# Kernel optimization log

Hardware: AMD Instinct MI355X
Metric: run time of the kernel (lower is better)

Reference implementation:

```python
import jax, jax.numpy as jnp
import numpy as np

P = 2048
D = 1024
H = 16
DH = D // H
HID = 32


def setup_inputs() -> dict:
    key = jax.random.key(0)
    ks = jax.random.split(key, 10)
    s = 0.02
    return {
        "x": jax.random.normal(ks[0], (P, D), jnp.float32),
        "rel": jax.random.normal(ks[1], (P, P, 2), jnp.float32),
        "w_qkv": jax.random.normal(ks[2], (D, 3 * D), jnp.float32) * s,
        "w_proj": jax.random.normal(ks[3], (D, D), jnp.float32) * s,
        "rpb_w1": jax.random.normal(ks[4], (2, HID), jnp.float32) * s,
        "rpb_b1": jnp.zeros((HID,), jnp.float32),
        "rpb_w2": jax.random.normal(ks[5], (HID, HID), jnp.float32) * s,
        "rpb_b2": jnp.zeros((HID,), jnp.float32),
        "rpb_w3": jax.random.normal(ks[6], (HID, 1), jnp.float32) * s,
        "rpb_b3": jnp.zeros((1,), jnp.float32),
    }


def reference(x, rel, w_qkv, w_proj, rpb_w1, rpb_b1, rpb_w2, rpb_b2, rpb_w3, rpb_b3):
    scale = 1.0 / np.sqrt(DH)
    qkv = x @ w_qkv                                   # [P, 3D]
    q, k, v = jnp.split(qkv, 3, axis=-1)
    # [P, D] -> [H, P, DH]
    q = q.reshape(P, H, DH).transpose(1, 0, 2)
    k = k.reshape(P, H, DH).transpose(1, 0, 2)
    v = v.reshape(P, H, DH).transpose(1, 0, 2)
    logits = jnp.einsum('hpd,hqd->hpq', q, k) * scale  # [H, P, P]
    # RelPosBias MLP: (dx,dy) -> scalar, applied over [P, P, 2]
    hcur = jax.nn.relu(rel @ rpb_w1 + rpb_b1)
    hcur = jax.nn.relu(hcur @ rpb_w2 + rpb_b2)
    bias = (hcur @ rpb_w3 + rpb_b3)[..., 0]            # [P, P]
    logits = logits + bias[None]
    attn = jax.nn.softmax(logits, axis=-1)
    out = jnp.einsum('hpq,hqd->hpd', attn, v)          # [H, P, DH]
    out = out.transpose(1, 0, 2).reshape(P, D)
    return out @ w_proj
```

## Files before the change

kernel.cpp:

```cpp
#include <hip/hip_runtime.h>
#include <hip/hip_bf16.h>
#include <type_traits>

typedef __attribute__((ext_vector_type(8))) short bf16x8;
typedef __attribute__((ext_vector_type(4))) float floatx4;
typedef __attribute__((ext_vector_type(2))) float float2v;

__device__ __forceinline__ float bf2f(unsigned short u) {
    union { unsigned int x; float f; } v; v.x = ((unsigned int)u) << 16; return v.f;
}
__device__ __forceinline__ unsigned short f2bf(float f) {
    union { float f; unsigned int u; } v; v.f = f;
    unsigned int x = v.u;
    unsigned int r = x + 0x7fffu + ((x >> 16) & 1u);
    return (unsigned short)(r >> 16);
}

typedef const __attribute__((address_space(1))) unsigned int u32_g;
typedef __attribute__((address_space(3))) unsigned int u32_l;
__device__ __forceinline__ void gld_lds16(const void* g, void* l) {
    __builtin_amdgcn_global_load_lds((u32_g*)g, (u32_l*)l, 16, 0, 0);
}

__device__ __forceinline__ void trans32(const float* __restrict__ in,
                                        unsigned short* __restrict__ out,
                                        int K, int N, int bx, int by,
                                        unsigned short (*T)[33]) {
    const int n0 = bx * 32, k0 = by * 32;
    const int r = threadIdx.x >> 3;
    const int c4 = (threadIdx.x & 7) * 4;
    float4 v = *reinterpret_cast<const float4*>(in + (size_t)(k0 + r) * N + n0 + c4);
    T[c4 + 0][r] = f2bf(v.x);
    T[c4 + 1][r] = f2bf(v.y);
    T[c4 + 2][r] = f2bf(v.z);
    T[c4 + 3][r] = f2bf(v.w);
    __syncthreads();
    ushort4 o = {T[r][c4], T[r][c4 + 1], T[r][c4 + 2], T[r][c4 + 3]};
    *reinterpret_cast<ushort4*>(out + (size_t)(n0 + r) * K + k0 + c4) = o;
}

__global__ __launch_bounds__(256) void prep(const float* __restrict__ x,
                                            unsigned short* __restrict__ xb,
                                            const float* __restrict__ wq,
                                            unsigned short* __restrict__ wqT,
                                            const float* __restrict__ wp,
                                            unsigned short* __restrict__ wpT) {
    __shared__ unsigned short T[32][33];
    const int b = blockIdx.x;
    if (b < 1024) {
        size_t i = ((size_t)b * 256 + threadIdx.x) * 8;
        float4 a = *reinterpret_cast<const float4*>(x + i);
        float4 c = *reinterpret_cast<const float4*>(x + i + 4);
        unsigned short t[8] = {f2bf(a.x), f2bf(a.y), f2bf(a.z), f2bf(a.w),
                               f2bf(c.x), f2bf(c.y), f2bf(c.z), f2bf(c.w)};
        *reinterpret_cast<uint4*>(xb + i) = *reinterpret_cast<const uint4*>(t);
    } else if (b < 4096) {
        int t = b - 1024;
        trans32(wq, wqT, 1024, 3072, t % 96, t / 96, T);
    } else {
        int t = b - 4096;
        trans32(wp, wpT, 1024, 1024, t % 32, t / 32, T);
    }
}

__device__ __forceinline__ void gemm128_body(const unsigned short* __restrict__ A,
                                             const unsigned short* __restrict__ Bt,
                                             unsigned short* __restrict__ C,
                                             int bx, int by,
                                             unsigned short* As, unsigned short* Bs) {
    const int tid = threadIdx.x;
    const int wave = tid >> 6;
    const int lane = tid & 63;
    const int m15 = lane & 15;
    const int quad = lane >> 4;
    const int wm = wave >> 1;
    const int wn = wave & 1;
    const int m0 = by * 128;
    const int n0 = bx * 128;
    const int srow = lane >> 2;
    const int scol = (lane & 3) * 8;

    floatx4 acc[4][4];
#pragma unroll
    for (int mt = 0; mt < 4; mt++)
#pragma unroll
        for (int nt = 0; nt < 4; nt++) acc[mt][nt] = {0.f, 0.f, 0.f, 0.f};

    for (int k0 = 0; k0 < 1024; k0 += 32) {
#pragma unroll
        for (int i = 0; i < 2; i++) {
            int j = wave * 2 + i;
            gld_lds16(A + (size_t)(m0 + j * 16 + srow) * 1024 + k0 + scol, &As[j * 16 * 32]);
            gld_lds16(Bt + (size_t)(n0 + j * 16 + srow) * 1024 + k0 + scol, &Bs[j * 16 * 32]);
        }
        __syncthreads();

        bf16x8 a[4];
#pragma unroll
        for (int mt = 0; mt < 4; mt++)
            a[mt] = *reinterpret_cast<bf16x8*>(&As[(wm * 64 + mt * 16 + m15) * 32 + quad * 8]);
#pragma unroll
        for (int nt = 0; nt < 4; nt++) {
            bf16x8 b = *reinterpret_cast<bf16x8*>(&Bs[(wn * 64 + nt * 16 + m15) * 32 + quad * 8]);
#pragma unroll
            for (int mt = 0; mt < 4; mt++)
                acc[mt][nt] = __builtin_amdgcn_mfma_f32_16x16x32_bf16(a[mt], b, acc[mt][nt], 0, 0, 0);
        }
        __syncthreads();
    }

#pragma unroll
    for (int mt = 0; mt < 4; mt++)
#pragma unroll
        for (int nt = 0; nt < 4; nt++)
#pragma unroll
            for (int i = 0; i < 4; i++) {
                int row = m0 + wm * 64 + mt * 16 + quad * 4 + i;
                int col = n0 + wn * 64 + nt * 16 + m15;
                C[(size_t)row * 3072 + col] = f2bf(acc[mt][nt][i]);
            }
}

__device__ __forceinline__ void rpb_body(int bx,
                                         const float* __restrict__ rel,
                                         const float* __restrict__ w1,
                                         const float* __restrict__ b1,
                                         const float* __restrict__ w2,
                                         const float* __restrict__ b2,
                                         const float* __restrict__ w3,
                                         const float* __restrict__ b3,
                                         unsigned short* __restrict__ biasb) {
    const int tid = threadIdx.x;
    const int wave = tid >> 6;
    const int lane = tid & 63;
    const int m15 = lane & 15;
    const int quad = lane >> 4;

    bf16x8 af0, af1;
    {
        unsigned short t0[8], t1[8];
#pragma unroll
        for (int j = 0; j < 8; j++) {
            int k = quad * 8 + j;
            t0[j] = f2bf(w2[k * 32 + m15]);
            t1[j] = f2bf(w2[k * 32 + 16 + m15]);
        }
        af0 = *reinterpret_cast<bf16x8*>(t0);
        af1 = *reinterpret_cast<bf16x8*>(t1);
    }

    float2v w1a2[4], w1b2[4], b12[4];
#pragma unroll
    for (int p = 0; p < 4; p++) {
        int base = quad * 8 + 2 * p;
        w1a2[p] = {w1[base], w1[base + 1]};
        w1b2[p] = {w1[32 + base], w1[32 + base + 1]};
        b12[p]  = {b1[base], b1[base + 1]};
    }

    floatx4 b2r0, b2r1;
    float2v w3p00, w3p01, w3p10, w3p11;
    const float LOG2E = 1.44269504f;
    {
        float4 t0 = *reinterpret_cast<const float4*>(b2 + quad * 4);
        float4 t1 = *reinterpret_cast<const float4*>(b2 + 16 + quad * 4);
        b2r0 = {t0.x, t0.y, t0.z, t0.w};
        b2r1 = {t1.x, t1.y, t1.z, t1.w};
        float4 u0 = *reinterpret_cast<const float4*>(w3 + quad * 4);
        float4 u1 = *reinterpret_cast<const float4*>(w3 + 16 + quad * 4);
        w3p00 = {u0.x * LOG2E, u0.y * LOG2E};
        w3p01 = {u0.z * LOG2E, u0.w * LOG2E};
        w3p10 = {u1.x * LOG2E, u1.y * LOG2E};
        w3p11 = {u1.z * LOG2E, u1.w * LOG2E};
    }
    const float b3s = b3[0] * LOG2E;
    const float2v z2 = {0.f, 0.f};
    const floatx4 b3r = {b3s, b3s, b3s, b3s};

    bf16x8 ones;
    {
        unsigned int t[4] = {0x3f803f80u, 0x3f803f80u, 0x3f803f80u, 0x3f803f80u};
        ones = *reinterpret_cast<bf16x8*>(t);
    }

    const int base = bx * 1024 + wave * 64;

    float2 cur[4];
#pragma unroll
    for (int t = 0; t < 4; t++)
        cur[t] = *reinterpret_cast<const float2*>(rel + (size_t)(base + t * 16 + m15) * 2);

    for (int it = 0; it < 4; ++it) {
        const int pix0 = base + it * 256;
        float2 nxt[4];
        if (it < 3) {
#pragma unroll
            for (int t = 0; t < 4; t++)
                nxt[t] = *reinterpret_cast<const float2*>(rel + (size_t)(pix0 + 256 + t * 16 + m15) * 2);
        }

#pragma unroll
        for (int t = 0; t < 4; t++) {
            float2v dx2 = {cur[t].x, cur[t].x}, dy2 = {cur[t].y, cur[t].y};

            unsigned int hp[4];
#pragma unroll
            for (int p = 0; p < 4; p++) {
                float2v h = __builtin_elementwise_fma(dx2, w1a2[p],
                             __builtin_elementwise_fma(dy2, w1b2[p], b12[p]));
                h = __builtin_elementwise_max(h, z2);
                hp[p] = __builtin_amdgcn_perm(__float_as_uint(h.y), __float_as_uint(h.x), 0x07060302u);
            }
            bf16x8 hb = *reinterpret_cast<bf16x8*>(hp);

            floatx4 d0 = __builtin_amdgcn_mfma_f32_16x16x32_bf16(af0, hb, b2r0, 0, 0, 0);
            floatx4 d1 = __builtin_amdgcn_mfma_f32_16x16x32_bf16(af1, hb, b2r1, 0, 0, 0);

            float2v m00 = __builtin_elementwise_max(__builtin_shufflevector(d0, d0, 0, 1), z2);
            float2v m01 = __builtin_elementwise_max(__builtin_shufflevector(d0, d0, 2, 3), z2);
            float2v m10 = __builtin_elementwise_max(__builtin_shufflevector(d1, d1, 0, 1), z2);
            float2v m11 = __builtin_elementwise_max(__builtin_shufflevector(d1, d1, 2, 3), z2);
            float2v acc2 = m00 * w3p00;
            acc2 = __builtin_elementwise_fma(m01, w3p01, acc2);
            acc2 = __builtin_elementwise_fma(m10, w3p10, acc2);
            acc2 = __builtin_elementwise_fma(m11, w3p11, acc2);
            float s = acc2.x + acc2.y;

            unsigned int sb[4];
            sb[0] = (unsigned int)f2bf(s);
            sb[1] = 0; sb[2] = 0; sb[3] = 0;
            bf16x8 sf = *reinterpret_cast<bf16x8*>(sb);
            floatx4 dsum = __builtin_amdgcn_mfma_f32_16x16x32_bf16(ones, sf, b3r, 0, 0, 0);

            if (quad == t)
                biasb[(size_t)pix0 + m15 * 4 + t] = f2bf(dsum[0]);
        }

        if (it < 3) {
#pragma unroll
            for (int t = 0; t < 4; t++) cur[t] = nxt[t];
        }
    }
}

__global__ __launch_bounds__(256) void gemm_rpb(const unsigned short* __restrict__ xb,
                                                const unsigned short* __restrict__ wqT,
                                                unsigned short* __restrict__ qkv,
                                                const float* __restrict__ rel,
                                                const float* __restrict__ w1,
                                                const float* __restrict__ b1,
                                                const float* __restrict__ w2,
                                                const float* __restrict__ b2,
                                                const float* __restrict__ w3,
                                                const float* __restrict__ b3,
                                                unsigned short* __restrict__ biasb) {
    __shared__ __align__(16) unsigned short S[2 * 128 * 32];
    const int b = blockIdx.x;
    if (b < 384)
        gemm128_body(xb, wqT, qkv, b % 24, b / 24, S, S + 128 * 32);
    else
        rpb_body(b - 384, rel, w1, b1, w2, b2, w3, b3, biasb);
}

template<int BN, typename TC>
__global__ __launch_bounds__(256) void gemm_abt(const unsigned short* __restrict__ A,
                                                const unsigned short* __restrict__ Bt,
                                                TC* __restrict__ C,
                                                int M, int N, int K) {
    constexpr int NT = BN / 32;
    __shared__ __align__(16) unsigned short As[64 * 32];
    __shared__ __align__(16) unsigned short Bs[BN * 32];

    const int tid = threadIdx.x;
    const int wave = tid >> 6;
    const int lane = tid & 63;
    const int m15 = lane & 15;
    const int quad = lane >> 4;
    const int wm = wave >> 1;
    const int wn = wave & 1;
    const int m0 = blockIdx.y * 64;
    const int n0 = blockIdx.x * BN;

    const int srow = lane >> 2;
    const int scol = (lane & 3) * 8;

    floatx4 acc[2][NT];
#pragma unroll
    for (int mt = 0; mt < 2; mt++)
#pragma unroll
        for (int nt = 0; nt < NT; nt++) acc[mt][nt] = {0.f, 0.f, 0.f, 0.f};

    for (int k0 = 0; k0 < K; k0 += 32) {
        gld_lds16(A + (size_t)(m0 + wave * 16 + srow) * K + k0 + scol, &As[wave * 16 * 32]);
#pragma unroll
        for (int i = 0; i < BN / 64; i++) {
            int j = wave * (BN / 64) + i;
            gld_lds16(Bt + (size_t)(n0 + j * 16 + srow) * K + k0 + scol, &Bs[j * 16 * 32]);
        }
        __syncthreads();

        bf16x8 a[2];
#pragma unroll
        for (int mt = 0; mt < 2; mt++)
            a[mt] = *reinterpret_cast<bf16x8*>(&As[(wm * 32 + mt * 16 + m15) * 32 + quad * 8]);
#pragma unroll
        for (int nt = 0; nt < NT; nt++) {
            bf16x8 b = *reinterpret_cast<bf16x8*>(&Bs[(wn * (BN / 2) + nt * 16 + m15) * 32 + quad * 8]);
#pragma unroll
            for (int mt = 0; mt < 2; mt++)
                acc[mt][nt] = __builtin_amdgcn_mfma_f32_16x16x32_bf16(a[mt], b, acc[mt][nt], 0, 0, 0);
        }
        __syncthreads();
    }

#pragma unroll
    for (int mt = 0; mt < 2; mt++)
#pragma unroll
        for (int nt = 0; nt < NT; nt++)
#pragma unroll
            for (int i = 0; i < 4; i++) {
                int row = m0 + wm * 32 + mt * 16 + quad * 4 + i;
                int col = n0 + wn * (BN / 2) + nt * 16 + m15;
                if constexpr (std::is_same<TC, float>::value)
                    C[(size_t)row * N + col] = acc[mt][nt][i];
                else
                    C[(size_t)row * N + col] = f2bf(acc[mt][nt][i]);
            }
}

__global__ __launch_bounds__(512, 4) void attn_kernel(const unsigned short* __restrict__ qkv,
                                                      const unsigned short* __restrict__ biasb,
                                                      unsigned short* __restrict__ attn_out) {
    const int h = blockIdx.x;
    const int q0 = blockIdx.y * 64;
    __shared__ __align__(16) unsigned short Kst[2][64 * 72];
    __shared__ __align__(16) unsigned short Vst[2][64 * 72];
    __shared__ __align__(16) unsigned short Ps[8][16 * 72];

    const int tid = threadIdx.x;
    const int g = tid >> 8;
    const int w = (tid >> 6) & 3;
    const int lane = tid & 63;
    const int ltid = tid & 255;
    const int m15 = lane & 15;
    const int quad = lane >> 4;

    bf16x8 qf[2];
#pragma unroll
    for (int kh = 0; kh < 2; kh++)
        qf[kh] = *reinterpret_cast<const bf16x8*>(
            qkv + (size_t)(q0 + w * 16 + m15) * 3072 + h * 64 + kh * 32 + quad * 8);

    const int kr0 = ltid >> 3, kd0 = (ltid & 7) * 8;
    const int ka = (ltid & 31) * 2;
    const int vd0 = (ltid >> 5) * 8;

    unsigned short* Kc = Kst[g];
    unsigned short* Vc = Vst[g];
    const size_t kofs = (size_t)g * 1024;

    uint4 kreg0 = *reinterpret_cast<const uint4*>(qkv + (kofs + kr0) * 3072 + 1024 + h * 64 + kd0);
    uint4 kreg1 = *reinterpret_cast<const uint4*>(qkv + (kofs + kr0 + 32) * 3072 + 1024 + h * 64 + kd0);
    uint4 vrega = *reinterpret_cast<const uint4*>(qkv + (kofs + ka) * 3072 + 2048 + h * 64 + vd0);
    uint4 vregb = *reinterpret_cast<const uint4*>(qkv + (kofs + ka + 1) * 3072 + 2048 + h * 64 + vd0);

    unsigned short br[16];
#pragma unroll
    for (int i = 0; i < 4; i++) {
        ushort4 t = *reinterpret_cast<const ushort4*>(
            biasb + (size_t)(q0 + w * 16 + quad * 4 + i) * 2048 + kofs + m15 * 4);
        br[0 * 4 + i] = t.x; br[1 * 4 + i] = t.y; br[2 * 4 + i] = t.z; br[3 * 4 + i] = t.w;
    }

    float rs[4] = {0.f, 0.f, 0.f, 0.f};
    floatx4 acc[4];
#pragma unroll
    for (int i = 0; i < 4; i++) acc[i] = {0.f, 0.f, 0.f, 0.f};
    const float c1 = 0.125f * 1.44269504f;

    for (int kt = 0; kt < 16; ++kt) {
        __syncthreads();

        *reinterpret_cast<uint4*>(&Kc[kr0 * 72 + kd0]) = kreg0;
        *reinterpret_cast<uint4*>(&Kc[(kr0 + 32) * 72 + kd0]) = kreg1;
        {
            const unsigned int* aw = reinterpret_cast<const unsigned int*>(&vrega);
            const unsigned int* bw = reinterpret_cast<const unsigned int*>(&vregb);
#pragma unroll
            for (int wd = 0; wd < 4; wd++) {
                unsigned int lo = __builtin_amdgcn_perm(bw[wd], aw[wd], 0x05040100u);
                unsigned int hi = __builtin_amdgcn_perm(bw[wd], aw[wd], 0x07060302u);
                *reinterpret_cast<unsigned int*>(&Vc[(vd0 + 2 * wd) * 72 + ka]) = lo;
                *reinterpret_cast<unsigned int*>(&Vc[(vd0 + 2 * wd + 1) * 72 + ka]) = hi;
            }
        }
        __syncthreads();

        if (kt < 15) {
            const size_t kb = kofs + (size_t)(kt + 1) * 64;
            kreg0 = *reinterpret_cast<const uint4*>(qkv + (kb + kr0) * 3072 + 1024 + h * 64 + kd0);
            kreg1 = *reinterpret_cast<const uint4*>(qkv + (kb + kr0 + 32) * 3072 + 1024 + h * 64 + kd0);
            vrega = *reinterpret_cast<const uint4*>(qkv + (kb + ka) * 3072 + 2048 + h * 64 + vd0);
            vregb = *reinterpret_cast<const uint4*>(qkv + (kb + ka + 1) * 3072 + 2048 + h * 64 + vd0);
        }

        floatx4 s[4];
#pragma unroll
        for (int nt = 0; nt < 4; nt++) s[nt] = {0.f, 0.f, 0.f, 0.f};
#pragma unroll
        for (int kh = 0; kh < 2; kh++) {
#pragma unroll
            for (int nt = 0; nt < 4; nt++) {
                bf16x8 b = *reinterpret_cast<bf16x8*>(&Kc[(nt * 16 + m15) * 72 + kh * 32 + quad * 8]);
                s[nt] = __builtin_amdgcn_mfma_f32_16x16x32_bf16(qf[kh], b, s[nt], 0, 0, 0);
            }
        }

        float p[4][4];
#pragma unroll
        for (int nt = 0; nt < 4; nt++)
#pragma unroll
            for (int i = 0; i < 4; i++) {
                float lg = fmaf(s[nt][i], c1, bf2f(br[nt * 4 + i]));
                p[nt][i] = __builtin_amdgcn_exp2f(lg);
                rs[i] += p[nt][i];
            }

        if (kt < 15) {
            const size_t kb = kofs + (size_t)(kt + 1) * 64;
#pragma unroll
            for (int i = 0; i < 4; i++) {
                ushort4 t = *reinterpret_cast<const ushort4*>(
                    biasb + (size_t)(q0 + w * 16 + quad * 4 + i) * 2048 + kb + m15 * 4);
                br[0 * 4 + i] = t.x; br[1 * 4 + i] = t.y; br[2 * 4 + i] = t.z; br[3 * 4 + i] = t.w;
            }
        }

        unsigned short* Pw = Ps[tid >> 6];
#pragma unroll
        for (int nt = 0; nt < 4; nt++)
#pragma unroll
            for (int i = 0; i < 4; i++)
                Pw[(quad * 4 + i) * 72 + nt * 16 + m15] = f2bf(p[nt][i]);
        __asm__ volatile("s_waitcnt lgkmcnt(0)" ::: "memory");

#pragma unroll
        for (int kh = 0; kh < 2; kh++) {
            bf16x8 a = *reinterpret_cast<bf16x8*>(&Pw[m15 * 72 + kh * 32 + quad * 8]);
#pragma unroll
            for (int nt = 0; nt < 4; nt++) {
                bf16x8 b = *reinterpret_cast<bf16x8*>(&Vc[(nt * 16 + m15) * 72 + kh * 32 + quad * 8]);
                acc[nt] = __builtin_amdgcn_mfma_f32_16x16x32_bf16(a, b, acc[nt], 0, 0, 0);
            }
        }
    }

    float rsum[4];
#pragma unroll
    for (int i = 0; i < 4; i++) {
        float r = rs[i];
        r += __shfl_xor(r, 1);
        r += __shfl_xor(r, 2);
        r += __shfl_xor(r, 4);
        r += __shfl_xor(r, 8);
        rsum[i] = r;
    }

    float* accbuf = reinterpret_cast<float*>(&Kst[0][0]);
    float* lbuf = accbuf + 4096;

    __syncthreads();
    if (g == 1) {
#pragma unroll
        for (int nt = 0; nt < 4; nt++)
#pragma unroll
            for (int i = 0; i < 4; i++)
                accbuf[(w * 16 + quad * 4 + i) * 64 + nt * 16 + m15] = acc[nt][i];
        if (m15 == 0) {
#pragma unroll
            for (int i = 0; i < 4; i++) lbuf[w * 16 + quad * 4 + i] = rsum[i];
        }
    }
    __syncthreads();
    if (g == 0) {
        float linv[4];
#pragma unroll
        for (int i = 0; i < 4; i++)
            linv[i] = 1.f / (rsum[i] + lbuf[w * 16 + quad * 4 + i]);
#pragma unroll
        for (int nt = 0; nt < 4; nt++)
#pragma unroll
            for (int i = 0; i < 4; i++) {
                float o = (acc[nt][i] + accbuf[(w * 16 + quad * 4 + i) * 64 + nt * 16 + m15]) * linv[i];
                int row = q0 + w * 16 + quad * 4 + i;
                int col = h * 64 + nt * 16 + m15;
                attn_out[(size_t)row * 1024 + col] = f2bf(o);
            }
    }
}

extern "C" void kernel_launch(void* const* d_in, const int* in_sizes, int n_in,
                              void* d_out, int out_size, void* d_ws, size_t ws_size,
                              hipStream_t stream) {
    const float* x      = (const float*)d_in[0];
    const float* rel    = (const float*)d_in[1];
    const float* w_qkv  = (const float*)d_in[2];
    const float* w_proj = (const float*)d_in[3];
    const float* w1     = (const float*)d_in[4];
    const float* b1     = (const float*)d_in[5];
    const float* w2     = (const float*)d_in[6];
    const float* b2     = (const float*)d_in[7];
    const float* w3     = (const float*)d_in[8];
    const float* b3     = (const float*)d_in[9];

    char* ws = (char*)d_ws;
    unsigned short* qkv   = (unsigned short*)ws;
    unsigned short* biasb = (unsigned short*)(ws + 12582912);
    unsigned short* xb    = (unsigned short*)(ws + 20971520);
    unsigned short* attn  = xb;
    unsigned short* wqT   = (unsigned short*)(ws + 25165824);
    unsigned short* wpT   = (unsigned short*)(ws + 31457280);
    float* out = (float*)d_out;

    prep<<<5120, 256, 0, stream>>>(x, xb, w_qkv, wqT, w_proj, wpT);
    gemm_rpb<<<4480, 256, 0, stream>>>(xb, wqT, qkv, rel, w1, b1, w2, b2, w3, b3, biasb);
    attn_kernel<<<dim3(16, 32), 512, 0, stream>>>(qkv, biasb, attn);
    gemm_abt<64, float><<<dim3(16, 32), 256, 0, stream>>>(attn, wpT, out, 2048, 1024, 1024);
}
```

Before: 211.9 us.

## Double-buffer GEMM LDS tiles, batch RPB reduction MFMA, add MFMA priority hints

Both bf16 GEMM bodies now keep two LDS buffers, so the global-to-LDS copy for the next K tile is issued before computing on the current one. This aims to hide load latency behind MFMA work and drop one barrier per iteration. In the RPB bias path, four per-pixel partial sums are packed into one MFMA with a selector matrix and written with a single vector store, replacing four MFMAs and four scalar stores. The attention kernel also raises wave priority around its MFMA blocks. Doubling LDS in the fused QKV/RPB kernel may lower occupancy.

New measurement: 208.8 us. Within noise of the previous version (-1.5%).

```diff
diff --git a/kernel.cpp b/kernel.cpp
--- a/kernel.cpp
+++ b/kernel.cpp
@@ -67,7 +67,7 @@
                                              const unsigned short* __restrict__ Bt,
                                              unsigned short* __restrict__ C,
                                              int bx, int by,
-                                             unsigned short* As, unsigned short* Bs) {
+                                             unsigned short* __restrict__ S) {
     const int tid = threadIdx.x;
     const int wave = tid >> 6;
     const int lane = tid & 63;
@@ -86,14 +86,25 @@
 #pragma unroll
         for (int nt = 0; nt < 4; nt++) acc[mt][nt] = {0.f, 0.f, 0.f, 0.f};
 
-    for (int k0 = 0; k0 < 1024; k0 += 32) {
+    auto stage = [&](int k0, unsigned short* As, unsigned short* Bs) {
 #pragma unroll
         for (int i = 0; i < 2; i++) {
             int j = wave * 2 + i;
             gld_lds16(A + (size_t)(m0 + j * 16 + srow) * 1024 + k0 + scol, &As[j * 16 * 32]);
             gld_lds16(Bt + (size_t)(n0 + j * 16 + srow) * 1024 + k0 + scol, &Bs[j * 16 * 32]);
         }
-        __syncthreads();
+    };
+
+    stage(0, S, S + 4096);
+    __syncthreads();
+
+    for (int kk = 0; kk < 32; ++kk) {
+        unsigned short* As = S + (kk & 1) * 8192;
+        unsigned short* Bs = As + 4096;
+        if (kk < 31) {
+            unsigned short* An = S + ((kk & 1) ^ 1) * 8192;
+            stage((kk + 1) * 32, An, An + 4096);
+        }
 
         bf16x8 a[4];
 #pragma unroll
@@ -177,10 +188,13 @@
     const float2v z2 = {0.f, 0.f};
     const floatx4 b3r = {b3s, b3s, b3s, b3s};
 
-    bf16x8 ones;
+    bf16x8 sel;
     {
-        unsigned int t[4] = {0x3f803f80u, 0x3f803f80u, 0x3f803f80u, 0x3f803f80u};
-        ones = *reinterpret_cast<bf16x8*>(t);
+        unsigned short t[8];
+#pragma unroll
+        for (int j = 0; j < 8; j++)
+            t[j] = (m15 == j) ? (unsigned short)0x3f80u : (unsigned short)0;
+        sel = *reinterpret_cast<bf16x8*>(t);
     }
 
     const int base = bx * 1024 + wave * 64;
@@ -199,6 +213,7 @@
                 nxt[t] = *reinterpret_cast<const float2*>(rel + (size_t)(pix0 + 256 + t * 16 + m15) * 2);
         }
 
+        float sreg[4];
 #pragma unroll
         for (int t = 0; t < 4; t++) {
             float2v dx2 = {cur[t].x, cur[t].x}, dy2 = {cur[t].y, cur[t].y};
@@ -224,16 +239,20 @@
             acc2 = __builtin_elementwise_fma(m01, w3p01, acc2);
             acc2 = __builtin_elementwise_fma(m10, w3p10, acc2);
             acc2 = __builtin_elementwise_fma(m11, w3p11, acc2);
-            float s = acc2.x + acc2.y;
-
-            unsigned int sb[4];
-            sb[0] = (unsigned int)f2bf(s);
-            sb[1] = 0; sb[2] = 0; sb[3] = 0;
-            bf16x8 sf = *reinterpret_cast<bf16x8*>(sb);
-            floatx4 dsum = __builtin_amdgcn_mfma_f32_16x16x32_bf16(ones, sf, b3r, 0, 0, 0);
-
-            if (quad == t)
-                biasb[(size_t)pix0 + m15 * 4 + t] = f2bf(dsum[0]);
+            sreg[t] = acc2.x + acc2.y;
+        }
+
+        unsigned int sb[4];
+        sb[0] = (unsigned int)f2bf(sreg[0]) | ((unsigned int)f2bf(sreg[1]) << 16);
+        sb[1] = (unsigned int)f2bf(sreg[2]) | ((unsigned int)f2bf(sreg[3]) << 16);
+        sb[2] = 0; sb[3] = 0;
+        bf16x8 sf = *reinterpret_cast<bf16x8*>(sb);
+        floatx4 dsum = __builtin_amdgcn_mfma_f32_16x16x32_bf16(sel, sf, b3r, 0, 0, 0);
+
+        if (quad == 0) {
+            unsigned short o[4] = {f2bf(dsum[0]), f2bf(dsum[1]), f2bf(dsum[2]), f2bf(dsum[3])};
+            *reinterpret_cast<ushort4*>(biasb + (size_t)pix0 + m15 * 4) =
+                *reinterpret_cast<const ushort4*>(o);
         }
 
         if (it < 3) {
@@ -254,10 +273,10 @@
                                                 const float* __restrict__ w3,
                                                 const float* __restrict__ b3,
                                                 unsigned short* __restrict__ biasb) {
-    __shared__ __align__(16) unsigned short S[2 * 128 * 32];
+    __shared__ __align__(16) unsigned short S[4 * 128 * 32];
     const int b = blockIdx.x;
     if (b < 384)
-        gemm128_body(xb, wqT, qkv, b % 24, b / 24, S, S + 128 * 32);
+        gemm128_body(xb, wqT, qkv, b % 24, b / 24, S);
     else
         rpb_body(b - 384, rel, w1, b1, w2, b2, w3, b3, biasb);
 }
@@ -268,8 +287,8 @@
                                                 TC* __restrict__ C,
                                                 int M, int N, int K) {
     constexpr int NT = BN / 32;
-    __shared__ __align__(16) unsigned short As[64 * 32];
-    __shared__ __align__(16) unsigned short Bs[BN * 32];
+    __shared__ __align__(16) unsigned short As[2][64 * 32];
+    __shared__ __align__(16) unsigned short Bs[2][BN * 32];
 
     const int tid = threadIdx.x;
     const int wave = tid >> 6;
@@ -290,22 +309,30 @@
 #pragma unroll
         for (int nt = 0; nt < NT; nt++) acc[mt][nt] = {0.f, 0.f, 0.f, 0.f};
 
-    for (int k0 = 0; k0 < K; k0 += 32) {
-        gld_lds16(A + (size_t)(m0 + wave * 16 + srow) * K + k0 + scol, &As[wave * 16 * 32]);
+    auto stage = [&](int k0, int buf) {
+        gld_lds16(A + (size_t)(m0 + wave * 16 + srow) * K + k0 + scol, &As[buf][wave * 16 * 32]);
 #pragma unroll
         for (int i = 0; i < BN / 64; i++) {
             int j = wave * (BN / 64) + i;
-            gld_lds16(Bt + (size_t)(n0 + j * 16 + srow) * K + k0 + scol, &Bs[j * 16 * 32]);
-        }
-        __syncthreads();
+            gld_lds16(Bt + (size_t)(n0 + j * 16 + srow) * K + k0 + scol, &Bs[buf][j * 16 * 32]);
+        }
+    };
+
+    const int nk = K >> 5;
+    stage(0, 0);
+    __syncthreads();
+
+    for (int kk = 0; kk < nk; ++kk) {
+        const int cur = kk & 1;
+        if (kk + 1 < nk) stage((kk + 1) * 32, cur ^ 1);
 
         bf16x8 a[2];
 #pragma unroll
         for (int mt = 0; mt < 2; mt++)
-            a[mt] = *reinterpret_cast<bf16x8*>(&As[(wm * 32 + mt * 16 + m15) * 32 + quad * 8]);
+            a[mt] = *reinterpret_cast<bf16x8*>(&As[cur][(wm * 32 + mt * 16 + m15) * 32 + quad * 8]);
 #pragma unroll
         for (int nt = 0; nt < NT; nt++) {
-            bf16x8 b = *reinterpret_cast<bf16x8*>(&Bs[(wn * (BN / 2) + nt * 16 + m15) * 32 + quad * 8]);
+            bf16x8 b = *reinterpret_cast<bf16x8*>(&Bs[cur][(wn * (BN / 2) + nt * 16 + m15) * 32 + quad * 8]);
 #pragma unroll
             for (int mt = 0; mt < 2; mt++)
                 acc[mt][nt] = __builtin_amdgcn_mfma_f32_16x16x32_bf16(a[mt], b, acc[mt][nt], 0, 0, 0);
@@ -407,6 +434,7 @@
         floatx4 s[4];
 #pragma unroll
         for (int nt = 0; nt < 4; nt++) s[nt] = {0.f, 0.f, 0.f, 0.f};
+        __builtin_amdgcn_s_setprio(1);
 #pragma unroll
         for (int kh = 0; kh < 2; kh++) {
 #pragma unroll
@@ -415,6 +443,7 @@
                 s[nt] = __builtin_amdgcn_mfma_f32_16x16x32_bf16(qf[kh], b, s[nt], 0, 0, 0);
             }
         }
+        __builtin_amdgcn_s_setprio(0);
 
         float p[4][4];
 #pragma unroll
@@ -444,6 +473,7 @@
                 Pw[(quad * 4 + i) * 72 + nt * 16 + m15] = f2bf(p[nt][i]);
         __asm__ volatile("s_waitcnt lgkmcnt(0)" ::: "memory");
 
+        __builtin_amdgcn_s_setprio(1);
 #pragma unroll
         for (int kh = 0; kh < 2; kh++) {
             bf16x8 a = *reinterpret_cast<bf16x8*>(&Pw[m15 * 72 + kh * 32 + quad * 8]);
@@ -453,6 +483,7 @@
                 acc[nt] = __builtin_amdgcn_mfma_f32_16x16x32_bf16(a, b, acc[nt], 0, 0, 0);
             }
         }
+        __builtin_amdgcn_s_setprio(0);
     }
 
     float rsum[4];
```
